# Performance work log

Measured on AMD Instinct MI355X. Metric: run time of the kernel, lower is better.

The kernel has to match this reference:

```python
import jax, jax.numpy as jnp
import numpy as np

N = 50000
E = 800000
D_IN = 128
D_HID = 128
D_OUT = 64
BN_EPS = 1e-5


def setup_inputs() -> dict:
    key = jax.random.key(0)
    ks = jax.random.split(key, 8)
    x = jax.random.normal(ks[0], (N, D_IN), dtype=jnp.float32)
    edge_index = jax.random.randint(ks[1], (2, E), 0, N, dtype=jnp.int64)
    # fc1
    W1 = jax.random.normal(ks[2], (D_IN, D_HID), dtype=jnp.float32) / np.sqrt(D_IN)
    b1 = jnp.zeros((D_HID,), dtype=jnp.float32)
    # bn1 affine params
    gamma = jnp.ones((D_HID,), dtype=jnp.float32)
    beta = jnp.zeros((D_HID,), dtype=jnp.float32)
    # fc2
    W2 = jax.random.normal(ks[3], (D_HID, D_OUT), dtype=jnp.float32) / np.sqrt(D_HID)
    b2 = jnp.zeros((D_OUT,), dtype=jnp.float32)
    return {"x": x, "W1": W1, "b1": b1, "gamma": gamma, "beta": beta,
            "W2": W2, "b2": b2, "edge_index": edge_index}


def _propagate(x, row, col):
    # add self loops for every node (reference convention)
    n = x.shape[0]
    sl = jnp.arange(n, dtype=row.dtype)
    row_f = jnp.concatenate([row, sl])
    col_f = jnp.concatenate([col, sl])
    # symmetric degree normalization: deg computed over destinations (col)
    deg = jax.ops.segment_sum(jnp.ones_like(col_f, dtype=x.dtype), col_f, num_segments=n)
    dis = deg ** -0.5
    w = dis[col_f] * dis[row_f]                       # [E+N]
    msg = w[:, None] * x[row_f]                       # [E+N, D] gather + scale
    return jax.ops.segment_sum(msg, col_f, num_segments=n)  # scatter-add


def reference(x, W1, b1, gamma, beta, W2, b2, edge_index):
    row, col = edge_index[0], edge_index[1]
    h = x @ W1 + b1                                   # [N, D_HID]
    h = _propagate(h, row, col)
    # BatchNorm1d with batch statistics (training-mode math, deterministic)
    mu = jnp.mean(h, axis=0)
    var = jnp.var(h, axis=0)
    h = (h - mu) * jax.lax.rsqrt(var + BN_EPS) * gamma + beta
    h = jax.nn.relu(h)
    # dropout treated as identity (eval) for a deterministic reference
    h = h @ W2 + b2                                   # [N, D_OUT]
    h = _propagate(h, row, col)
    return jax.nn.log_softmax(h, axis=1)
```

## Files before the change

### kernel.cpp

```cpp
#include <hip/hip_runtime.h>
#include <hip/hip_bf16.h>

#define N_NODES 50000
#define NE      800000
#define DIN     128
#define DHID    128
#define DOUT    64
#define BN_EPS  1e-5f
#define SLOT    64
#define NBUK    196
#define BCAP    4864
#define EPB     2048
#define NPART   32
#define LDW     132
#define LDW2    132

typedef __hip_bfloat16 bf16;
typedef short bf16x8 __attribute__((ext_vector_type(8)));
typedef float f32x4 __attribute__((ext_vector_type(4)));

__device__ __forceinline__ float ldf(const void* p, int i, int isbf) {
    if (isbf) return __bfloat162float(((const bf16*)p)[i]);
    return ((const float*)p)[i];
}
__device__ __forceinline__ unsigned short f2b(float f) {
    bf16 h = __float2bfloat16(f);
    return *(unsigned short*)&h;
}
__device__ __forceinline__ float2 up2(unsigned int u) {
    return make_float2(__uint_as_float(u << 16), __uint_as_float(u & 0xffff0000u));
}
__device__ __forceinline__ unsigned int pk2(float a, float b) {
    return ((unsigned int)f2b(a)) | (((unsigned int)f2b(b)) << 16);
}

#define DETECT_ISBF(W1raw, tid, sdet, isbf_out)                                   \
    if ((tid) == 0) sdet = 0;                                                     \
    __syncthreads();                                                              \
    {                                                                             \
        unsigned int u_ = ((unsigned int)((const unsigned short*)(W1raw))[tid]) << 16; \
        float f_ = fabsf(__uint_as_float(u_));                                    \
        if (!isnan(f_) && !isinf(f_) && f_ > 1e4f) atomicOr(&sdet, 1);            \
    }                                                                             \
    __syncthreads();                                                              \
    const int isbf_out = !sdet;

__global__ __launch_bounds__(256) void k_binA(const void* eiraw, int* __restrict__ gcnt,
                                              unsigned int* __restrict__ bpk) {
    __shared__ int hist[256], scanb[256], eofs[256], cur[256], gbase[256];
    __shared__ unsigned int stg[EPB];
    __shared__ int sdet;
    int tid = threadIdx.x;
    if (tid == 0) sdet = 0;
    hist[tid] = 0;
    __syncthreads();
    if (tid < 64 && ((const unsigned int*)eiraw)[2 * tid + 1] != 0u) atomicOr(&sdet, 1);
    __syncthreads();
    const int isll = !sdet;

    int e0 = blockIdx.x * EPB;
    int nE = NE - e0; if (nE > EPB) nE = EPB;
    int r[8], c[8];
    #pragma unroll
    for (int q = 0; q < 8; ++q) {
        int li = q * 256 + tid;
        if (li < nE) {
            int e = e0 + li;
            if (isll) { r[q] = (int)((const long long*)eiraw)[e]; c[q] = (int)((const long long*)eiraw)[NE + e]; }
            else      { r[q] = ((const int*)eiraw)[e];            c[q] = ((const int*)eiraw)[NE + e]; }
            atomicAdd(&hist[c[q] >> 8], 1);
        } else r[q] = -1;
    }
    __syncthreads();
    int hv = hist[tid];
    scanb[tid] = hv;
    __syncthreads();
    for (int off = 1; off < 256; off <<= 1) {
        int u = (tid >= off) ? scanb[tid - off] : 0;
        __syncthreads();
        scanb[tid] += u;
        __syncthreads();
    }
    int ex = scanb[tid] - hv;
    eofs[tid] = ex;
    cur[tid] = ex;
    if (tid < NBUK) gbase[tid] = atomicAdd(&gcnt[tid], hv);
    __syncthreads();
    #pragma unroll
    for (int q = 0; q < 8; ++q) {
        if (r[q] >= 0) {
            int b = c[q] >> 8;
            int p = atomicAdd(&cur[b], 1);
            stg[p] = ((unsigned int)b << 24) | ((unsigned int)(c[q] & 255) << 16) | (unsigned int)r[q];
        }
    }
    __syncthreads();
    for (int i = tid; i < nE; i += 256) {
        unsigned int v = stg[i];
        int b = v >> 24;
        int pos = gbase[b] + (i - eofs[b]);
        if (pos < BCAP) bpk[(size_t)b * BCAP + pos] = v;
    }
}

__global__ __launch_bounds__(256) void k_binB(const unsigned int* __restrict__ bpk, const int* __restrict__ gcnt,
                                              int* __restrict__ counts, int* __restrict__ ej) {
    __shared__ int cnt[256], scanb[256], eofs[256], cur[256];
    __shared__ unsigned int stg[BCAP];
    int b = blockIdx.x;
    int tid = threadIdx.x;
    int m = gcnt[b]; if (m > BCAP) m = BCAP;
    cnt[tid] = 0;
    __syncthreads();
    const unsigned int* src = bpk + (size_t)b * BCAP;
    for (int i = tid; i < m; i += 256)
        atomicAdd(&cnt[(src[i] >> 16) & 255], 1);
    __syncthreads();
    int hv = cnt[tid];
    scanb[tid] = hv;
    __syncthreads();
    for (int off = 1; off < 256; off <<= 1) {
        int u = (tid >= off) ? scanb[tid - off] : 0;
        __syncthreads();
        scanb[tid] += u;
        __syncthreads();
    }
    int ex = scanb[tid] - hv;
    eofs[tid] = ex;
    cur[tid] = ex;
    __syncthreads();
    for (int i = tid; i < m; i += 256) {
        unsigned int v = src[i];
        int cl = (v >> 16) & 255;
        int p = atomicAdd(&cur[cl], 1);
        stg[p] = v & 0x00ffffffu;
    }
    __syncthreads();
    int c0 = b << 8;
    int cg = c0 + tid;
    if (cg < N_NODES) {
        counts[cg] = hv;
        int hc = hv < SLOT ? hv : SLOT;
        int hp = (hc + 15) & ~15; if (hp > SLOT) hp = SLOT;
        for (int k = hc; k < hp; ++k) ej[(size_t)cg * SLOT + k] = N_NODES;
    }
    for (int i = tid; i < m; i += 256) {
        unsigned int v = stg[i];
        int cl = v >> 16;
        int k = i - eofs[cl];
        if (k < SLOT) ej[(size_t)(c0 + cl) * SLOT + k] = (int)(v & 0xffffu);
    }
}

__global__ __launch_bounds__(256) void k_gemm1_mfma(const void* __restrict__ x, const void* __restrict__ W1,
                                                    const void* __restrict__ b1, const int* __restrict__ counts,
                                                    unsigned short* __restrict__ g1) {
    __shared__ unsigned short wt[128 * LDW];
    __shared__ int sdet;
    int tid = threadIdx.x;
    DETECT_ISBF(W1, tid, sdet, isbf)

    #pragma unroll 4
    for (int i = 0; i < 64; ++i) {
        int idx = i * 256 + tid;
        int k = idx >> 7, n = idx & 127;
        wt[n * LDW + k] = isbf ? ((const unsigned short*)W1)[idx]
                               : f2b(((const float*)W1)[idx]);
    }
    __syncthreads();

    int lane = tid & 63;
    int wave = tid >> 6;
    int m0 = blockIdx.x * 64 + wave * 16;
    int lm = lane & 15;
    int quad = lane >> 4;

    bf16x8 a[4];
    int arow = m0 + lm;
    int arow_c = arow < N_NODES ? arow : 0;
    if (isbf) {
        const unsigned short* xb = (const unsigned short*)x;
        #pragma unroll
        for (int q = 0; q < 4; ++q)
            a[q] = *(const bf16x8*)(xb + arow_c * DIN + q * 32 + quad * 8);
    } else {
        const float* xf = (const float*)x;
        #pragma unroll
        for (int q = 0; q < 4; ++q) {
            bf16x8 t;
            #pragma unroll
            for (int j = 0; j < 8; ++j)
                t[j] = (short)f2b(xf[arow_c * DIN + q * 32 + quad * 8 + j]);
            a[q] = t;
        }
    }

    float dsc[4];
    #pragma unroll
    for (int r = 0; r < 4; ++r) {
        int grow = m0 + quad * 4 + r;
        dsc[r] = (grow < N_NODES) ? rsqrtf((float)(counts[grow] + 1)) : 0.f;
    }

    #pragma unroll
    for (int nt = 0; nt < 8; ++nt) {
        int n0 = nt * 16;
        f32x4 acc = {0.f, 0.f, 0.f, 0.f};
        #pragma unroll
        for (int q = 0; q < 4; ++q) {
            bf16x8 b = *(const bf16x8*)(wt + (n0 + lm) * LDW + q * 32 + quad * 8);
            acc = __builtin_amdgcn_mfma_f32_16x16x32_bf16(a[q], b, acc, 0, 0, 0);
        }
        float bias = ldf(b1, n0 + lm, isbf);
        #pragma unroll
        for (int r = 0; r < 4; ++r) {
            int grow = m0 + quad * 4 + r;
            if (grow <= N_NODES)
                g1[grow * DHID + n0 + lm] = f2b(dsc[r] * (acc[r] + bias));
        }
    }
}

__global__ __launch_bounds__(256) void k_prop1(const int* __restrict__ counts, const int* __restrict__ ej,
                                               const unsigned int* __restrict__ g1p,
                                               unsigned int* __restrict__ agg1p,
                                               float* __restrict__ statsP) {
    __shared__ float sp[1024];
    int tid = threadIdx.x;
    int w = tid >> 6;
    int n = blockIdx.x * 4 + w;
    n = __builtin_amdgcn_readfirstlane(n);
    int lane = tid & 63;
    float ax = 0.f, ay = 0.f;
    if (n < N_NODES) {
        int cnt = counts[n];
        int t = cnt < SLOT ? cnt : SLOT;
        int tp = (t + 15) & ~15; if (tp > SLOT) tp = SLOT;
        const int* ejn = ej + (size_t)n * SLOT;
        float2 v = up2(g1p[(size_t)n * 64 + lane]);
        float ax0 = v.x, ay0 = v.y, ax1 = 0.f, ay1 = 0.f;
        float ax2 = 0.f, ay2 = 0.f, ax3 = 0.f, ay3 = 0.f;
        for (int j = 0; j < tp; j += 16) {
            const int4* ej4 = (const int4*)(ejn + j);
            int4 E0 = ej4[0], E1 = ej4[1], E2 = ej4[2], E3 = ej4[3];
            int e[16] = {E0.x, E0.y, E0.z, E0.w, E1.x, E1.y, E1.z, E1.w,
                         E2.x, E2.y, E2.z, E2.w, E3.x, E3.y, E3.z, E3.w};
            unsigned int gg[16];
            #pragma unroll
            for (int q = 0; q < 16; ++q) gg[q] = g1p[(size_t)e[q] * 64 + lane];
            #pragma unroll
            for (int q = 0; q < 16; ++q) {
                float2 f = up2(gg[q]);
                if ((q & 3) == 0) { ax0 += f.x; ay0 += f.y; }
                else if ((q & 3) == 1) { ax1 += f.x; ay1 += f.y; }
                else if ((q & 3) == 2) { ax2 += f.x; ay2 += f.y; }
                else { ax3 += f.x; ay3 += f.y; }
            }
        }
        float dv = rsqrtf((float)(cnt + 1));
        ax = dv * ((ax0 + ax1) + (ax2 + ax3));
        ay = dv * ((ay0 + ay1) + (ay2 + ay3));
        agg1p[(size_t)n * 64 + lane] = pk2(ax, ay);
    }
    sp[w * 256 + 2 * lane]       = ax;
    sp[w * 256 + 2 * lane + 1]   = ay;
    sp[w * 256 + 128 + 2 * lane] = ax * ax;
    sp[w * 256 + 129 + 2 * lane] = ay * ay;
    __syncthreads();
    float s = sp[tid] + sp[256 + tid] + sp[512 + tid] + sp[768 + tid];
    atomicAdd(&statsP[(blockIdx.x & (NPART - 1)) * 256 + tid], s);
}

__global__ __launch_bounds__(256) void k_gemm2_mfma(const unsigned int* __restrict__ agg1p,
                                                    const float* __restrict__ statsP,
                                                    const void* __restrict__ gamma, const void* __restrict__ beta,
                                                    const void* __restrict__ W2, const void* __restrict__ b2,
                                                    const void* __restrict__ W1, const int* __restrict__ counts,
                                                    unsigned short* __restrict__ g2) {
    __shared__ unsigned short w2t[64 * LDW2];
    __shared__ float sc[128], sh[128], redu[256];
    __shared__ int sdet;
    int tid = threadIdx.x;
    DETECT_ISBF(W1, tid, sdet, isbf)

    #pragma unroll 4
    for (int i = 0; i < 32; ++i) {
        int idx = i * 256 + tid;
        int k = idx >> 6, n = idx & 63;
        w2t[n * LDW2 + k] = isbf ? ((const unsigned short*)W2)[idx]
                                 : f2b(((const float*)W2)[idx]);
    }
    {
        float s = 0.f;
        #pragma unroll
        for (int p = 0; p < NPART; ++p) s += statsP[p * 256 + tid];
        redu[tid] = s;
    }
    __syncthreads();
    if (tid < 128) {
        const float invn = 1.0f / (float)N_NODES;
        float mu = redu[tid] * invn;
        float var = redu[128 + tid] * invn - mu * mu;
        float rs = rsqrtf(var + BN_EPS);
        float g = ldf(gamma, tid, isbf);
        sc[tid] = rs * g;
        sh[tid] = ldf(beta, tid, isbf) - mu * rs * g;
    }
    __syncthreads();

    int lane = tid & 63;
    int wave = tid >> 6;
    int m0 = blockIdx.x * 64 + wave * 16;
    int lm = lane & 15;
    int quad = lane >> 4;

    int arow = m0 + lm;
    int arow_c = arow < N_NODES ? arow : 0;
    bf16x8 a[4];
    #pragma unroll
    for (int q = 0; q < 4; ++q) {
        uint4 gv = *(const uint4*)(agg1p + (size_t)arow_c * 64 + q * 16 + quad * 4);
        int kb = q * 32 + quad * 8;
        float2 f0 = up2(gv.x), f1 = up2(gv.y), f2 = up2(gv.z), f3 = up2(gv.w);
        float e0 = f0.x * sc[kb + 0] + sh[kb + 0];
        float e1 = f0.y * sc[kb + 1] + sh[kb + 1];
        float e2 = f1.x * sc[kb + 2] + sh[kb + 2];
        float e3 = f1.y * sc[kb + 3] + sh[kb + 3];
        float e4 = f2.x * sc[kb + 4] + sh[kb + 4];
        float e5 = f2.y * sc[kb + 5] + sh[kb + 5];
        float e6 = f3.x * sc[kb + 6] + sh[kb + 6];
        float e7 = f3.y * sc[kb + 7] + sh[kb + 7];
        bf16x8 t;
        t[0] = (short)f2b(e0 > 0.f ? e0 : 0.f);
        t[1] = (short)f2b(e1 > 0.f ? e1 : 0.f);
        t[2] = (short)f2b(e2 > 0.f ? e2 : 0.f);
        t[3] = (short)f2b(e3 > 0.f ? e3 : 0.f);
        t[4] = (short)f2b(e4 > 0.f ? e4 : 0.f);
        t[5] = (short)f2b(e5 > 0.f ? e5 : 0.f);
        t[6] = (short)f2b(e6 > 0.f ? e6 : 0.f);
        t[7] = (short)f2b(e7 > 0.f ? e7 : 0.f);
        a[q] = t;
    }

    float dsc[4];
    #pragma unroll
    for (int r = 0; r < 4; ++r) {
        int grow = m0 + quad * 4 + r;
        dsc[r] = (grow < N_NODES) ? rsqrtf((float)(counts[grow] + 1)) : 0.f;
    }

    #pragma unroll
    for (int nt = 0; nt < 4; ++nt) {
        int n0 = nt * 16;
        f32x4 acc = {0.f, 0.f, 0.f, 0.f};
        #pragma unroll
        for (int q = 0; q < 4; ++q) {
            bf16x8 b = *(const bf16x8*)(w2t + (n0 + lm) * LDW2 + q * 32 + quad * 8);
            acc = __builtin_amdgcn_mfma_f32_16x16x32_bf16(a[q], b, acc, 0, 0, 0);
        }
        float bias = ldf(b2, n0 + lm, isbf);
        #pragma unroll
        for (int r = 0; r < 4; ++r) {
            int grow = m0 + quad * 4 + r;
            if (grow <= N_NODES)
                g2[grow * DOUT + n0 + lm] = f2b(dsc[r] * (acc[r] + bias));
        }
    }
}

__global__ __launch_bounds__(256) void k_prop2_lsm(const int* __restrict__ counts, const int* __restrict__ ej,
                                                   const unsigned int* __restrict__ g2p,
                                                   const void* __restrict__ W1, void* __restrict__ out) {
    __shared__ int sdet;
    int tid = threadIdx.x;
    DETECT_ISBF(W1, tid, sdet, isbf)

    int n = blockIdx.x * 8 + (tid >> 5);
    if (n >= N_NODES) return;
    int lane = tid & 31;
    int cnt = counts[n];
    int t = cnt < SLOT ? cnt : SLOT;
    int tp = (t + 15) & ~15; if (tp > SLOT) tp = SLOT;
    const int* ejn = ej + (size_t)n * SLOT;
    float2 v = up2(g2p[(size_t)n * 32 + lane]);
    float ax0 = v.x, ay0 = v.y, ax1 = 0.f, ay1 = 0.f;
    float ax2 = 0.f, ay2 = 0.f, ax3 = 0.f, ay3 = 0.f;
    for (int j = 0; j < tp; j += 16) {
        const int4* ej4 = (const int4*)(ejn + j);
        int4 E0 = ej4[0], E1 = ej4[1], E2 = ej4[2], E3 = ej4[3];
        int e[16] = {E0.x, E0.y, E0.z, E0.w, E1.x, E1.y, E1.z, E1.w,
                     E2.x, E2.y, E2.z, E2.w, E3.x, E3.y, E3.z, E3.w};
        unsigned int gg[16];
        #pragma unroll
        for (int q = 0; q < 16; ++q) gg[q] = g2p[(size_t)e[q] * 32 + lane];
        #pragma unroll
        for (int q = 0; q < 16; ++q) {
            float2 f = up2(gg[q]);
            if ((q & 3) == 0) { ax0 += f.x; ay0 += f.y; }
            else if ((q & 3) == 1) { ax1 += f.x; ay1 += f.y; }
            else if ((q & 3) == 2) { ax2 += f.x; ay2 += f.y; }
            else { ax3 += f.x; ay3 += f.y; }
        }
    }
    float dv = rsqrtf((float)(cnt + 1));
    float ax = dv * ((ax0 + ax1) + (ax2 + ax3));
    float ay = dv * ((ay0 + ay1) + (ay2 + ay3));
    float m = fmaxf(ax, ay);
    #pragma unroll
    for (int off = 16; off >= 1; off >>= 1) m = fmaxf(m, __shfl_xor(m, off, 32));
    float sum = __expf(ax - m) + __expf(ay - m);
    #pragma unroll
    for (int off = 16; off >= 1; off >>= 1) sum += __shfl_xor(sum, off, 32);
    float lse = m + __logf(sum);
    float rx = ax - lse, ry = ay - lse;
    if (isbf) {
        ((unsigned int*)out)[(size_t)n * 32 + lane] = pk2(rx, ry);
    } else {
        float2* o = (float2*)((float*)out + (size_t)n * 64 + 2 * lane);
        *o = make_float2(rx, ry);
    }
}

extern "C" void kernel_launch(void* const* d_in, const int* in_sizes, int n_in,
                              void* d_out, int out_size, void* d_ws, size_t ws_size,
                              hipStream_t stream) {
    const void* x     = d_in[0];
    const void* W1    = d_in[1];
    const void* b1    = d_in[2];
    const void* gamma = d_in[3];
    const void* beta  = d_in[4];
    const void* W2    = d_in[5];
    const void* b2    = d_in[6];
    const void* ei    = d_in[7];

    char* w = (char*)d_ws;
    float*          statsP = (float*)(w + 0);
    int*            gcnt   = (int*)(w + 32768);
    int*            counts = (int*)(w + 33792);
    int*            ej     = (int*)(w + 233792);
    unsigned int*   bpk    = (unsigned int*)(w + 13033792);
    unsigned short* g1     = (unsigned short*)(w + 16847168);
    unsigned int*   agg1p  = (unsigned int*)(w + 29647424);
    unsigned short* g2     = (unsigned short*)(w + 42447424);

    hipMemsetAsync(w, 0, 33792, stream);

    k_binA<<<(NE + EPB - 1) / EPB, 256, 0, stream>>>(ei, gcnt, bpk);
    k_binB<<<NBUK, 256, 0, stream>>>(bpk, gcnt, counts, ej);

    k_gemm1_mfma<<<(N_NODES + 63) / 64, 256, 0, stream>>>(x, W1, b1, counts, g1);

    k_prop1<<<(N_NODES + 3) / 4, 256, 0, stream>>>(counts, ej, (const unsigned int*)g1, agg1p, statsP);

    k_gemm2_mfma<<<(N_NODES + 63) / 64, 256, 0, stream>>>(agg1p, statsP, gamma, beta, W2, b2,
                                                          W1, counts, g2);

    k_prop2_lsm<<<(N_NODES + 7) / 8, 256, 0, stream>>>(counts, ej, (const unsigned int*)g2, W1, d_out);
}
```

Before: 216.2 us.

## Pad edge slots to 32 and unroll gathers fully; gemm1 processes two row tiles per block

The edge-list padding now always fills at least 32 slots, so the propagation kernels issue all 32 neighbour gathers at once with no loop, plus a second fixed block of 32 when the degree exceeds 32. This is meant to raise memory-level parallelism and remove loop overhead for the typical degree of about 16. In exchange, nodes with few neighbours gather more padding entries that point at the zero row. gemm1 now covers 128 rows per block, which halves the number of blocks that each reload and transpose W1 into shared memory.

New measurement: 220.5 us. 1.02x slower.

```diff
diff --git a/kernel.cpp b/kernel.cpp
--- a/kernel.cpp
+++ b/kernel.cpp
@@ -141,7 +141,7 @@
     if (cg < N_NODES) {
         counts[cg] = hv;
         int hc = hv < SLOT ? hv : SLOT;
-        int hp = (hc + 15) & ~15; if (hp > SLOT) hp = SLOT;
+        int hp = (hc <= 32) ? 32 : SLOT;
         for (int k = hc; k < hp; ++k) ej[(size_t)cg * SLOT + k] = N_NODES;
     }
     for (int i = tid; i < m; i += 256) {
@@ -171,52 +171,55 @@
 
     int lane = tid & 63;
     int wave = tid >> 6;
-    int m0 = blockIdx.x * 64 + wave * 16;
     int lm = lane & 15;
     int quad = lane >> 4;
 
-    bf16x8 a[4];
-    int arow = m0 + lm;
-    int arow_c = arow < N_NODES ? arow : 0;
-    if (isbf) {
-        const unsigned short* xb = (const unsigned short*)x;
-        #pragma unroll
-        for (int q = 0; q < 4; ++q)
-            a[q] = *(const bf16x8*)(xb + arow_c * DIN + q * 32 + quad * 8);
-    } else {
-        const float* xf = (const float*)x;
-        #pragma unroll
-        for (int q = 0; q < 4; ++q) {
-            bf16x8 t;
-            #pragma unroll
-            for (int j = 0; j < 8; ++j)
-                t[j] = (short)f2b(xf[arow_c * DIN + q * 32 + quad * 8 + j]);
-            a[q] = t;
-        }
-    }
-
-    float dsc[4];
-    #pragma unroll
-    for (int r = 0; r < 4; ++r) {
-        int grow = m0 + quad * 4 + r;
-        dsc[r] = (grow < N_NODES) ? rsqrtf((float)(counts[grow] + 1)) : 0.f;
-    }
-
-    #pragma unroll
-    for (int nt = 0; nt < 8; ++nt) {
-        int n0 = nt * 16;
-        f32x4 acc = {0.f, 0.f, 0.f, 0.f};
-        #pragma unroll
-        for (int q = 0; q < 4; ++q) {
-            bf16x8 b = *(const bf16x8*)(wt + (n0 + lm) * LDW + q * 32 + quad * 8);
-            acc = __builtin_amdgcn_mfma_f32_16x16x32_bf16(a[q], b, acc, 0, 0, 0);
-        }
-        float bias = ldf(b1, n0 + lm, isbf);
+    for (int half = 0; half < 2; ++half) {
+        int m0 = blockIdx.x * 128 + half * 64 + wave * 16;
+
+        bf16x8 a[4];
+        int arow = m0 + lm;
+        int arow_c = arow < N_NODES ? arow : 0;
+        if (isbf) {
+            const unsigned short* xb = (const unsigned short*)x;
+            #pragma unroll
+            for (int q = 0; q < 4; ++q)
+                a[q] = *(const bf16x8*)(xb + arow_c * DIN + q * 32 + quad * 8);
+        } else {
+            const float* xf = (const float*)x;
+            #pragma unroll
+            for (int q = 0; q < 4; ++q) {
+                bf16x8 t;
+                #pragma unroll
+                for (int j = 0; j < 8; ++j)
+                    t[j] = (short)f2b(xf[arow_c * DIN + q * 32 + quad * 8 + j]);
+                a[q] = t;
+            }
+        }
+
+        float dsc[4];
         #pragma unroll
         for (int r = 0; r < 4; ++r) {
             int grow = m0 + quad * 4 + r;
-            if (grow <= N_NODES)
-                g1[grow * DHID + n0 + lm] = f2b(dsc[r] * (acc[r] + bias));
+            dsc[r] = (grow < N_NODES) ? rsqrtf((float)(counts[grow] + 1)) : 0.f;
+        }
+
+        #pragma unroll
+        for (int nt = 0; nt < 8; ++nt) {
+            int n0 = nt * 16;
+            f32x4 acc = {0.f, 0.f, 0.f, 0.f};
+            #pragma unroll
+            for (int q = 0; q < 4; ++q) {
+                bf16x8 b = *(const bf16x8*)(wt + (n0 + lm) * LDW + q * 32 + quad * 8);
+                acc = __builtin_amdgcn_mfma_f32_16x16x32_bf16(a[q], b, acc, 0, 0, 0);
+            }
+            float bias = ldf(b1, n0 + lm, isbf);
+            #pragma unroll
+            for (int r = 0; r < 4; ++r) {
+                int grow = m0 + quad * 4 + r;
+                if (grow <= N_NODES)
+                    g1[grow * DHID + n0 + lm] = f2b(dsc[r] * (acc[r] + bias));
+            }
         }
     }
 }
@@ -235,26 +238,41 @@
     if (n < N_NODES) {
         int cnt = counts[n];
         int t = cnt < SLOT ? cnt : SLOT;
-        int tp = (t + 15) & ~15; if (tp > SLOT) tp = SLOT;
         const int* ejn = ej + (size_t)n * SLOT;
         float2 v = up2(g1p[(size_t)n * 64 + lane]);
         float ax0 = v.x, ay0 = v.y, ax1 = 0.f, ay1 = 0.f;
         float ax2 = 0.f, ay2 = 0.f, ax3 = 0.f, ay3 = 0.f;
-        for (int j = 0; j < tp; j += 16) {
-            const int4* ej4 = (const int4*)(ejn + j);
-            int4 E0 = ej4[0], E1 = ej4[1], E2 = ej4[2], E3 = ej4[3];
-            int e[16] = {E0.x, E0.y, E0.z, E0.w, E1.x, E1.y, E1.z, E1.w,
-                         E2.x, E2.y, E2.z, E2.w, E3.x, E3.y, E3.z, E3.w};
-            unsigned int gg[16];
-            #pragma unroll
-            for (int q = 0; q < 16; ++q) gg[q] = g1p[(size_t)e[q] * 64 + lane];
-            #pragma unroll
-            for (int q = 0; q < 16; ++q) {
+        {
+            const int4* ej4 = (const int4*)ejn;
+            int4 E[8];
+            #pragma unroll
+            for (int q = 0; q < 8; ++q) E[q] = ej4[q];
+            int e[32];
+            #pragma unroll
+            for (int q = 0; q < 8; ++q) { e[4*q] = E[q].x; e[4*q+1] = E[q].y; e[4*q+2] = E[q].z; e[4*q+3] = E[q].w; }
+            unsigned int gg[32];
+            #pragma unroll
+            for (int q = 0; q < 32; ++q) gg[q] = g1p[(size_t)e[q] * 64 + lane];
+            #pragma unroll
+            for (int q = 0; q < 32; ++q) {
                 float2 f = up2(gg[q]);
                 if ((q & 3) == 0) { ax0 += f.x; ay0 += f.y; }
                 else if ((q & 3) == 1) { ax1 += f.x; ay1 += f.y; }
                 else if ((q & 3) == 2) { ax2 += f.x; ay2 += f.y; }
                 else { ax3 += f.x; ay3 += f.y; }
+            }
+        }
+        if (t > 32) {
+            const int4* ej4 = (const int4*)(ejn + 32);
+            #pragma unroll
+            for (int qq = 0; qq < 8; ++qq) {
+                int4 E = ej4[qq];
+                float2 f0 = up2(g1p[(size_t)E.x * 64 + lane]);
+                float2 f1 = up2(g1p[(size_t)E.y * 64 + lane]);
+                float2 f2 = up2(g1p[(size_t)E.z * 64 + lane]);
+                float2 f3 = up2(g1p[(size_t)E.w * 64 + lane]);
+                ax0 += f0.x; ay0 += f0.y; ax1 += f1.x; ay1 += f1.y;
+                ax2 += f2.x; ay2 += f2.y; ax3 += f3.x; ay3 += f3.y;
             }
         }
         float dv = rsqrtf((float)(cnt + 1));
@@ -380,26 +398,41 @@
     int lane = tid & 31;
     int cnt = counts[n];
     int t = cnt < SLOT ? cnt : SLOT;
-    int tp = (t + 15) & ~15; if (tp > SLOT) tp = SLOT;
     const int* ejn = ej + (size_t)n * SLOT;
     float2 v = up2(g2p[(size_t)n * 32 + lane]);
     float ax0 = v.x, ay0 = v.y, ax1 = 0.f, ay1 = 0.f;
     float ax2 = 0.f, ay2 = 0.f, ax3 = 0.f, ay3 = 0.f;
-    for (int j = 0; j < tp; j += 16) {
-        const int4* ej4 = (const int4*)(ejn + j);
-        int4 E0 = ej4[0], E1 = ej4[1], E2 = ej4[2], E3 = ej4[3];
-        int e[16] = {E0.x, E0.y, E0.z, E0.w, E1.x, E1.y, E1.z, E1.w,
-                     E2.x, E2.y, E2.z, E2.w, E3.x, E3.y, E3.z, E3.w};
-        unsigned int gg[16];
-        #pragma unroll
-        for (int q = 0; q < 16; ++q) gg[q] = g2p[(size_t)e[q] * 32 + lane];
-        #pragma unroll
-        for (int q = 0; q < 16; ++q) {
+    {
+        const int4* ej4 = (const int4*)ejn;
+        int4 E[8];
+        #pragma unroll
+        for (int q = 0; q < 8; ++q) E[q] = ej4[q];
+        int e[32];
+        #pragma unroll
+        for (int q = 0; q < 8; ++q) { e[4*q] = E[q].x; e[4*q+1] = E[q].y; e[4*q+2] = E[q].z; e[4*q+3] = E[q].w; }
+        unsigned int gg[32];
+        #pragma unroll
+        for (int q = 0; q < 32; ++q) gg[q] = g2p[(size_t)e[q] * 32 + lane];
+        #pragma unroll
+        for (int q = 0; q < 32; ++q) {
             float2 f = up2(gg[q]);
             if ((q & 3) == 0) { ax0 += f.x; ay0 += f.y; }
             else if ((q & 3) == 1) { ax1 += f.x; ay1 += f.y; }
             else if ((q & 3) == 2) { ax2 += f.x; ay2 += f.y; }
             else { ax3 += f.x; ay3 += f.y; }
+        }
+    }
+    if (t > 32) {
+        const int4* ej4 = (const int4*)(ejn + 32);
+        #pragma unroll
+        for (int qq = 0; qq < 8; ++qq) {
+            int4 E = ej4[qq];
+            float2 f0 = up2(g2p[(size_t)E.x * 32 + lane]);
+            float2 f1 = up2(g2p[(size_t)E.y * 32 + lane]);
+            float2 f2 = up2(g2p[(size_t)E.z * 32 + lane]);
+            float2 f3 = up2(g2p[(size_t)E.w * 32 + lane]);
+            ax0 += f0.x; ay0 += f0.y; ax1 += f1.x; ay1 += f1.y;
+            ax2 += f2.x; ay2 += f2.y; ax3 += f3.x; ay3 += f3.y;
         }
     }
     float dv = rsqrtf((float)(cnt + 1));
@@ -448,7 +481,7 @@
     k_binA<<<(NE + EPB - 1) / EPB, 256, 0, stream>>>(ei, gcnt, bpk);
     k_binB<<<NBUK, 256, 0, stream>>>(bpk, gcnt, counts, ej);
 
-    k_gemm1_mfma<<<(N_NODES + 63) / 64, 256, 0, stream>>>(x, W1, b1, counts, g1);
+    k_gemm1_mfma<<<(N_NODES + 127) / 128, 256, 0, stream>>>(x, W1, b1, counts, g1);
 
     k_prop1<<<(N_NODES + 3) / 4, 256, 0, stream>>>(counts, ej, (const unsigned int*)g1, agg1p, statsP);
 
```

## Fuse edge binning with first GEMM and move source normalization into propagation

Applied to the files above, without the earlier changes.

The first GEMM no longer needs node degrees, so it is merged into the edge-binning launch as extra blocks that run alongside the binning blocks. This removes one kernel launch and lets the dense GEMM overlap with the binning work. The degree normalization of source nodes moves from the GEMM epilogue into prop1, which now gathers a precomputed per-node dis vector (written by binB) for each neighbor. That adds a second random gather per edge in prop1 in exchange for the overlap, and it grows the workspace layout.

Result: no change. 218.7 us (+1.1%).

```diff
diff --git a/kernel.cpp b/kernel.cpp
--- a/kernel.cpp
+++ b/kernel.cpp
@@ -14,6 +14,8 @@
 #define NPART   32
 #define LDW     132
 #define LDW2    132
+#define BINA_BLOCKS ((NE + EPB - 1) / EPB)
+#define G1_BLOCKS   ((N_NODES + 63) / 64)
 
 typedef __hip_bfloat16 bf16;
 typedef short bf16x8 __attribute__((ext_vector_type(8)));
@@ -45,66 +47,138 @@
     __syncthreads();                                                              \
     const int isbf_out = !sdet;
 
-__global__ __launch_bounds__(256) void k_binA(const void* eiraw, int* __restrict__ gcnt,
-                                              unsigned int* __restrict__ bpk) {
-    __shared__ int hist[256], scanb[256], eofs[256], cur[256], gbase[256];
-    __shared__ unsigned int stg[EPB];
+__global__ __launch_bounds__(256) void k_binA_gemm1(const void* eiraw, int* __restrict__ gcnt,
+                                                    unsigned int* __restrict__ bpk,
+                                                    const void* __restrict__ x, const void* __restrict__ W1,
+                                                    const void* __restrict__ b1,
+                                                    unsigned short* __restrict__ g1) {
+    __shared__ __align__(16) char smraw[33792];
     __shared__ int sdet;
     int tid = threadIdx.x;
-    if (tid == 0) sdet = 0;
-    hist[tid] = 0;
-    __syncthreads();
-    if (tid < 64 && ((const unsigned int*)eiraw)[2 * tid + 1] != 0u) atomicOr(&sdet, 1);
-    __syncthreads();
-    const int isll = !sdet;
-
-    int e0 = blockIdx.x * EPB;
-    int nE = NE - e0; if (nE > EPB) nE = EPB;
-    int r[8], c[8];
-    #pragma unroll
-    for (int q = 0; q < 8; ++q) {
-        int li = q * 256 + tid;
-        if (li < nE) {
-            int e = e0 + li;
-            if (isll) { r[q] = (int)((const long long*)eiraw)[e]; c[q] = (int)((const long long*)eiraw)[NE + e]; }
-            else      { r[q] = ((const int*)eiraw)[e];            c[q] = ((const int*)eiraw)[NE + e]; }
-            atomicAdd(&hist[c[q] >> 8], 1);
-        } else r[q] = -1;
-    }
-    __syncthreads();
-    int hv = hist[tid];
-    scanb[tid] = hv;
-    __syncthreads();
-    for (int off = 1; off < 256; off <<= 1) {
-        int u = (tid >= off) ? scanb[tid - off] : 0;
-        __syncthreads();
-        scanb[tid] += u;
-        __syncthreads();
-    }
-    int ex = scanb[tid] - hv;
-    eofs[tid] = ex;
-    cur[tid] = ex;
-    if (tid < NBUK) gbase[tid] = atomicAdd(&gcnt[tid], hv);
-    __syncthreads();
-    #pragma unroll
-    for (int q = 0; q < 8; ++q) {
-        if (r[q] >= 0) {
-            int b = c[q] >> 8;
-            int p = atomicAdd(&cur[b], 1);
-            stg[p] = ((unsigned int)b << 24) | ((unsigned int)(c[q] & 255) << 16) | (unsigned int)r[q];
-        }
-    }
-    __syncthreads();
-    for (int i = tid; i < nE; i += 256) {
-        unsigned int v = stg[i];
-        int b = v >> 24;
-        int pos = gbase[b] + (i - eofs[b]);
-        if (pos < BCAP) bpk[(size_t)b * BCAP + pos] = v;
+
+    if (blockIdx.x < BINA_BLOCKS) {
+        int* hist  = (int*)smraw;
+        int* scanb = hist + 256;
+        int* eofs  = scanb + 256;
+        int* cur   = eofs + 256;
+        int* gbase = cur + 256;
+        unsigned int* stg = (unsigned int*)(gbase + 256);
+
+        if (tid == 0) sdet = 0;
+        hist[tid] = 0;
+        __syncthreads();
+        if (tid < 64 && ((const unsigned int*)eiraw)[2 * tid + 1] != 0u) atomicOr(&sdet, 1);
+        __syncthreads();
+        const int isll = !sdet;
+
+        int e0 = blockIdx.x * EPB;
+        int nE = NE - e0; if (nE > EPB) nE = EPB;
+        int r[8], c[8];
+        #pragma unroll
+        for (int q = 0; q < 8; ++q) {
+            int li = q * 256 + tid;
+            if (li < nE) {
+                int e = e0 + li;
+                if (isll) { r[q] = (int)((const long long*)eiraw)[e]; c[q] = (int)((const long long*)eiraw)[NE + e]; }
+                else      { r[q] = ((const int*)eiraw)[e];            c[q] = ((const int*)eiraw)[NE + e]; }
+                atomicAdd(&hist[c[q] >> 8], 1);
+            } else r[q] = -1;
+        }
+        __syncthreads();
+        int hv = hist[tid];
+        scanb[tid] = hv;
+        __syncthreads();
+        for (int off = 1; off < 256; off <<= 1) {
+            int u = (tid >= off) ? scanb[tid - off] : 0;
+            __syncthreads();
+            scanb[tid] += u;
+            __syncthreads();
+        }
+        int ex = scanb[tid] - hv;
+        eofs[tid] = ex;
+        cur[tid] = ex;
+        if (tid < NBUK) gbase[tid] = atomicAdd(&gcnt[tid], hv);
+        __syncthreads();
+        #pragma unroll
+        for (int q = 0; q < 8; ++q) {
+            if (r[q] >= 0) {
+                int b = c[q] >> 8;
+                int p = atomicAdd(&cur[b], 1);
+                stg[p] = ((unsigned int)b << 24) | ((unsigned int)(c[q] & 255) << 16) | (unsigned int)r[q];
+            }
+        }
+        __syncthreads();
+        for (int i = tid; i < nE; i += 256) {
+            unsigned int v = stg[i];
+            int b = v >> 24;
+            int pos = gbase[b] + (i - eofs[b]);
+            if (pos < BCAP) bpk[(size_t)b * BCAP + pos] = v;
+        }
+    } else {
+        unsigned short* wt = (unsigned short*)smraw;
+        DETECT_ISBF(W1, tid, sdet, isbf)
+
+        #pragma unroll 4
+        for (int i = 0; i < 64; ++i) {
+            int idx = i * 256 + tid;
+            int k = idx >> 7, n = idx & 127;
+            wt[n * LDW + k] = isbf ? ((const unsigned short*)W1)[idx]
+                                   : f2b(((const float*)W1)[idx]);
+        }
+        __syncthreads();
+
+        int lane = tid & 63;
+        int wave = tid >> 6;
+        int bid = blockIdx.x - BINA_BLOCKS;
+        int m0 = bid * 64 + wave * 16;
+        int lm = lane & 15;
+        int quad = lane >> 4;
+
+        bf16x8 a[4];
+        int arow = m0 + lm;
+        int arow_c = arow < N_NODES ? arow : 0;
+        if (isbf) {
+            const unsigned short* xb = (const unsigned short*)x;
+            #pragma unroll
+            for (int q = 0; q < 4; ++q)
+                a[q] = *(const bf16x8*)(xb + arow_c * DIN + q * 32 + quad * 8);
+        } else {
+            const float* xf = (const float*)x;
+            #pragma unroll
+            for (int q = 0; q < 4; ++q) {
+                bf16x8 t;
+                #pragma unroll
+                for (int j = 0; j < 8; ++j)
+                    t[j] = (short)f2b(xf[arow_c * DIN + q * 32 + quad * 8 + j]);
+                a[q] = t;
+            }
+        }
+
+        #pragma unroll
+        for (int nt = 0; nt < 8; ++nt) {
+            int n0 = nt * 16;
+            f32x4 acc = {0.f, 0.f, 0.f, 0.f};
+            #pragma unroll
+            for (int q = 0; q < 4; ++q) {
+                bf16x8 b = *(const bf16x8*)(wt + (n0 + lm) * LDW + q * 32 + quad * 8);
+                acc = __builtin_amdgcn_mfma_f32_16x16x32_bf16(a[q], b, acc, 0, 0, 0);
+            }
+            float bias = ldf(b1, n0 + lm, isbf);
+            #pragma unroll
+            for (int r = 0; r < 4; ++r) {
+                int grow = m0 + quad * 4 + r;
+                if (grow <= N_NODES) {
+                    float val = (grow < N_NODES) ? (acc[r] + bias) : 0.f;
+                    g1[grow * DHID + n0 + lm] = f2b(val);
+                }
+            }
+        }
     }
 }
 
 __global__ __launch_bounds__(256) void k_binB(const unsigned int* __restrict__ bpk, const int* __restrict__ gcnt,
-                                              int* __restrict__ counts, int* __restrict__ ej) {
+                                              int* __restrict__ counts, float* __restrict__ disv,
+                                              int* __restrict__ ej) {
     __shared__ int cnt[256], scanb[256], eofs[256], cur[256];
     __shared__ unsigned int stg[BCAP];
     int b = blockIdx.x;
@@ -140,9 +214,12 @@
     int cg = c0 + tid;
     if (cg < N_NODES) {
         counts[cg] = hv;
+        disv[cg] = rsqrtf((float)(hv + 1));
         int hc = hv < SLOT ? hv : SLOT;
         int hp = (hc + 15) & ~15; if (hp > SLOT) hp = SLOT;
         for (int k = hc; k < hp; ++k) ej[(size_t)cg * SLOT + k] = N_NODES;
+    } else if (cg == N_NODES) {
+        disv[cg] = 0.f;
     }
     for (int i = tid; i < m; i += 256) {
         unsigned int v = stg[i];
@@ -152,76 +229,8 @@
     }
 }
 
-__global__ __launch_bounds__(256) void k_gemm1_mfma(const void* __restrict__ x, const void* __restrict__ W1,
-                                                    const void* __restrict__ b1, const int* __restrict__ counts,
-                                                    unsigned short* __restrict__ g1) {
-    __shared__ unsigned short wt[128 * LDW];
-    __shared__ int sdet;
-    int tid = threadIdx.x;
-    DETECT_ISBF(W1, tid, sdet, isbf)
-
-    #pragma unroll 4
-    for (int i = 0; i < 64; ++i) {
-        int idx = i * 256 + tid;
-        int k = idx >> 7, n = idx & 127;
-        wt[n * LDW + k] = isbf ? ((const unsigned short*)W1)[idx]
-                               : f2b(((const float*)W1)[idx]);
-    }
-    __syncthreads();
-
-    int lane = tid & 63;
-    int wave = tid >> 6;
-    int m0 = blockIdx.x * 64 + wave * 16;
-    int lm = lane & 15;
-    int quad = lane >> 4;
-
-    bf16x8 a[4];
-    int arow = m0 + lm;
-    int arow_c = arow < N_NODES ? arow : 0;
-    if (isbf) {
-        const unsigned short* xb = (const unsigned short*)x;
-        #pragma unroll
-        for (int q = 0; q < 4; ++q)
-            a[q] = *(const bf16x8*)(xb + arow_c * DIN + q * 32 + quad * 8);
-    } else {
-        const float* xf = (const float*)x;
-        #pragma unroll
-        for (int q = 0; q < 4; ++q) {
-            bf16x8 t;
-            #pragma unroll
-            for (int j = 0; j < 8; ++j)
-                t[j] = (short)f2b(xf[arow_c * DIN + q * 32 + quad * 8 + j]);
-            a[q] = t;
-        }
-    }
-
-    float dsc[4];
-    #pragma unroll
-    for (int r = 0; r < 4; ++r) {
-        int grow = m0 + quad * 4 + r;
-        dsc[r] = (grow < N_NODES) ? rsqrtf((float)(counts[grow] + 1)) : 0.f;
-    }
-
-    #pragma unroll
-    for (int nt = 0; nt < 8; ++nt) {
-        int n0 = nt * 16;
-        f32x4 acc = {0.f, 0.f, 0.f, 0.f};
-        #pragma unroll
-        for (int q = 0; q < 4; ++q) {
-            bf16x8 b = *(const bf16x8*)(wt + (n0 + lm) * LDW + q * 32 + quad * 8);
-            acc = __builtin_amdgcn_mfma_f32_16x16x32_bf16(a[q], b, acc, 0, 0, 0);
-        }
-        float bias = ldf(b1, n0 + lm, isbf);
-        #pragma unroll
-        for (int r = 0; r < 4; ++r) {
-            int grow = m0 + quad * 4 + r;
-            if (grow <= N_NODES)
-                g1[grow * DHID + n0 + lm] = f2b(dsc[r] * (acc[r] + bias));
-        }
-    }
-}
-
-__global__ __launch_bounds__(256) void k_prop1(const int* __restrict__ counts, const int* __restrict__ ej,
+__global__ __launch_bounds__(256) void k_prop1(const int* __restrict__ counts, const float* __restrict__ disv,
+                                               const int* __restrict__ ej,
                                                const unsigned int* __restrict__ g1p,
                                                unsigned int* __restrict__ agg1p,
                                                float* __restrict__ statsP) {
@@ -234,11 +243,12 @@
     float ax = 0.f, ay = 0.f;
     if (n < N_NODES) {
         int cnt = counts[n];
+        float dv = disv[n];
         int t = cnt < SLOT ? cnt : SLOT;
         int tp = (t + 15) & ~15; if (tp > SLOT) tp = SLOT;
         const int* ejn = ej + (size_t)n * SLOT;
         float2 v = up2(g1p[(size_t)n * 64 + lane]);
-        float ax0 = v.x, ay0 = v.y, ax1 = 0.f, ay1 = 0.f;
+        float ax0 = dv * v.x, ay0 = dv * v.y, ax1 = 0.f, ay1 = 0.f;
         float ax2 = 0.f, ay2 = 0.f, ax3 = 0.f, ay3 = 0.f;
         for (int j = 0; j < tp; j += 16) {
             const int4* ej4 = (const int4*)(ejn + j);
@@ -246,18 +256,18 @@
             int e[16] = {E0.x, E0.y, E0.z, E0.w, E1.x, E1.y, E1.z, E1.w,
                          E2.x, E2.y, E2.z, E2.w, E3.x, E3.y, E3.z, E3.w};
             unsigned int gg[16];
-            #pragma unroll
-            for (int q = 0; q < 16; ++q) gg[q] = g1p[(size_t)e[q] * 64 + lane];
+            float ds[16];
+            #pragma unroll
+            for (int q = 0; q < 16; ++q) { gg[q] = g1p[(size_t)e[q] * 64 + lane]; ds[q] = disv[e[q]]; }
             #pragma unroll
             for (int q = 0; q < 16; ++q) {
                 float2 f = up2(gg[q]);
-                if ((q & 3) == 0) { ax0 += f.x; ay0 += f.y; }
-                else if ((q & 3) == 1) { ax1 += f.x; ay1 += f.y; }
-                else if ((q & 3) == 2) { ax2 += f.x; ay2 += f.y; }
-                else { ax3 += f.x; ay3 += f.y; }
+                if ((q & 3) == 0) { ax0 = fmaf(ds[q], f.x, ax0); ay0 = fmaf(ds[q], f.y, ay0); }
+                else if ((q & 3) == 1) { ax1 = fmaf(ds[q], f.x, ax1); ay1 = fmaf(ds[q], f.y, ay1); }
+                else if ((q & 3) == 2) { ax2 = fmaf(ds[q], f.x, ax2); ay2 = fmaf(ds[q], f.y, ay2); }
+                else { ax3 = fmaf(ds[q], f.x, ax3); ay3 = fmaf(ds[q], f.y, ay3); }
             }
         }
-        float dv = rsqrtf((float)(cnt + 1));
         ax = dv * ((ax0 + ax1) + (ax2 + ax3));
         ay = dv * ((ay0 + ay1) + (ay2 + ay3));
         agg1p[(size_t)n * 64 + lane] = pk2(ax, ay);
@@ -437,20 +447,20 @@
     float*          statsP = (float*)(w + 0);
     int*            gcnt   = (int*)(w + 32768);
     int*            counts = (int*)(w + 33792);
-    int*            ej     = (int*)(w + 233792);
-    unsigned int*   bpk    = (unsigned int*)(w + 13033792);
-    unsigned short* g1     = (unsigned short*)(w + 16847168);
-    unsigned int*   agg1p  = (unsigned int*)(w + 29647424);
-    unsigned short* g2     = (unsigned short*)(w + 42447424);
+    float*          disv   = (float*)(w + 233792);
+    int*            ej     = (int*)(w + 433808);
+    unsigned int*   bpk    = (unsigned int*)(w + 13233808);
+    unsigned short* g1     = (unsigned short*)(w + 17047184);
+    unsigned int*   agg1p  = (unsigned int*)(w + 29847440);
+    unsigned short* g2     = (unsigned short*)(w + 42647440);
 
     hipMemsetAsync(w, 0, 33792, stream);
 
-    k_binA<<<(NE + EPB - 1) / EPB, 256, 0, stream>>>(ei, gcnt, bpk);
-    k_binB<<<NBUK, 256, 0, stream>>>(bpk, gcnt, counts, ej);
-
-    k_gemm1_mfma<<<(N_NODES + 63) / 64, 256, 0, stream>>>(x, W1, b1, counts, g1);
-
-    k_prop1<<<(N_NODES + 3) / 4, 256, 0, stream>>>(counts, ej, (const unsigned int*)g1, agg1p, statsP);
+    k_binA_gemm1<<<BINA_BLOCKS + G1_BLOCKS, 256, 0, stream>>>(ei, gcnt, bpk, x, W1, b1, g1);
+
+    k_binB<<<NBUK, 256, 0, stream>>>(bpk, gcnt, counts, disv, ej);
+
+    k_prop1<<<(N_NODES + 3) / 4, 256, 0, stream>>>(counts, disv, ej, (const unsigned int*)g1, agg1p, statsP);
 
     k_gemm2_mfma<<<(N_NODES + 63) / 64, 256, 0, stream>>>(agg1p, statsP, gamma, beta, W2, b2,
                                                           W1, counts, g2);
```
